# Kernel tuning notes

Measured on AMD Instinct MI355X. Metric: run time of the kernel, lower is better.

## Reference

```python
import jax, jax.numpy as jnp
import numpy as np

N_KV_HEADS = 8
MAX_CONTEXT = 8192
HEAD_DIM = 128  # dim // n_heads = 4096 // 32
N_NEW = 16


def setup_inputs() -> dict:
    key = jax.random.key(0)
    k1, k2, k3, k4, k5 = jax.random.split(key, 5)
    pos_ids = jnp.sort(jax.random.randint(k1, (N_NEW,), 0, MAX_CONTEXT, dtype=jnp.int64))
    k = jax.random.normal(k2, (1, N_KV_HEADS, N_NEW, HEAD_DIM), dtype=jnp.float32)
    v = jax.random.normal(k3, (1, N_KV_HEADS, N_NEW, HEAD_DIM), dtype=jnp.float32)
    k_cache = jax.random.normal(k4, (1, N_KV_HEADS, MAX_CONTEXT, HEAD_DIM), dtype=jnp.float32)
    v_cache = jax.random.normal(k5, (1, N_KV_HEADS, MAX_CONTEXT, HEAD_DIM), dtype=jnp.float32)
    return {"pos_ids": pos_ids, "k": k, "v": v, "k_cache": k_cache, "v_cache": v_cache}


def reference(pos_ids, k, v, k_cache, v_cache):
    # Functional equivalent of: clone cache, then cache[:, :, pos_ids, :] = new.
    # jnp .at[].set on the seq axis produces a fresh (copied) buffer, matching
    # the torch clone-then-scatter semantics.
    kout = k_cache.at[:, :, pos_ids, :].set(k)
    vout = v_cache.at[:, :, pos_ids, :].set(v)
    return (kout, vout)
```

## Files before the change

kernel.cpp:

```cpp
#include <hip/hip_runtime.h>


#define NNEW 16

typedef float f32x4 __attribute__((ext_vector_type(4)));

__global__ __launch_bounds__(256) void kv_copy_kernel(
    const f32x4* __restrict__ kcache,
    const f32x4* __restrict__ vcache,
    f32x4* __restrict__ out)
{
    const unsigned int i = blockIdx.x * 256u + threadIdx.x;
    const unsigned int j = i & ((1u << 21) - 1u);
    const f32x4* __restrict__ src = (i >> 21) ? vcache : kcache;
    f32x4 val = __builtin_nontemporal_load(&src[j]);
    __builtin_nontemporal_store(val, &out[i]);
}

__global__ __launch_bounds__(256) void kv_scatter_kernel(
    const int* __restrict__ pos,
    const f32x4* __restrict__ knew,
    const f32x4* __restrict__ vnew,
    f32x4* __restrict__ out)
{
    const unsigned int t  = blockIdx.x * 256u + threadIdx.x;
    const unsigned int d4 = t & 31u;
    const unsigned int n  = (t >> 5) & 15u;
    const unsigned int h  = (t >> 9) & 7u;
    const unsigned int c  = t >> 12;

    const int s = pos[n];

    bool skip = false;
#pragma unroll
    for (int m = 0; m < NNEW; ++m) {
        if (m > (int)n && pos[m] == s) skip = true;
    }
    if (skip) return;

    const f32x4* __restrict__ src = c ? vnew : knew;
    out[(c << 21) + (h << 18) + ((unsigned)s << 5) + d4] =
        src[(h * NNEW + n) * 32u + d4];
}

extern "C" void kernel_launch(void* const* d_in, const int* in_sizes, int n_in,
                              void* d_out, int out_size, void* d_ws, size_t ws_size,
                              hipStream_t stream) {
    const int*   pos    = (const int*)  d_in[0];
    const f32x4* knew   = (const f32x4*)d_in[1];
    const f32x4* vnew   = (const f32x4*)d_in[2];
    const f32x4* kcache = (const f32x4*)d_in[3];
    const f32x4* vcache = (const f32x4*)d_in[4];
    f32x4*       out    = (f32x4*)d_out;

    kv_copy_kernel<<<(1u << 22) / 256u, 256, 0, stream>>>(kcache, vcache, out);
    kv_scatter_kernel<<<8192 / 256, 256, 0, stream>>>(pos, knew, vnew, out);
}
```

Baseline: 128.3 us.

## Fuse cache copy and scatter into one kernel with per-row position lookup

Merges the bulk copy kernel and the scatter kernel into a single launch. Each thread owns four 16-byte chunks of one cache row, checks whether that row's sequence index matches any new position (the last match wins), and copies from either the new k/v or the old cache. This removes the second launch and avoids writing the new rows twice, but every thread now scans the 16-entry position list and the nontemporal load/store hints are dropped.

```diff
diff --git a/kernel.cpp b/kernel.cpp
--- a/kernel.cpp
+++ b/kernel.cpp
@@ -5,42 +5,48 @@
 
 typedef float f32x4 __attribute__((ext_vector_type(4)));
 
-__global__ __launch_bounds__(256) void kv_copy_kernel(
+__global__ __launch_bounds__(256) void kv_update_kernel(
+    const int* __restrict__ pos,
+    const f32x4* __restrict__ knew,
+    const f32x4* __restrict__ vnew,
     const f32x4* __restrict__ kcache,
     const f32x4* __restrict__ vcache,
     f32x4* __restrict__ out)
 {
-    const unsigned int i = blockIdx.x * 256u + threadIdx.x;
-    const unsigned int j = i & ((1u << 21) - 1u);
-    const f32x4* __restrict__ src = (i >> 21) ? vcache : kcache;
-    f32x4 val = __builtin_nontemporal_load(&src[j]);
-    __builtin_nontemporal_store(val, &out[i]);
-}
+    const unsigned int t  = blockIdx.x * 256u + threadIdx.x;
+    const unsigned int c  = t >> 19;
+    const unsigned int jb = t & ((1u << 19) - 1u);
+    const unsigned int r  = jb >> 3;
+    const unsigned int g  = jb & 7u;
+    const unsigned int h  = r >> 13;
+    const int          s  = (int)(r & 8191u);
 
-__global__ __launch_bounds__(256) void kv_scatter_kernel(
-    const int* __restrict__ pos,
-    const f32x4* __restrict__ knew,
-    const f32x4* __restrict__ vnew,
-    f32x4* __restrict__ out)
-{
-    const unsigned int t  = blockIdx.x * 256u + threadIdx.x;
-    const unsigned int d4 = t & 31u;
-    const unsigned int n  = (t >> 5) & 15u;
-    const unsigned int h  = (t >> 9) & 7u;
-    const unsigned int c  = t >> 12;
+    int match = -1;
+#pragma unroll
+    for (int n = 0; n < NNEW; ++n) {
+        if (pos[n] == s) match = n;
+    }
 
-    const int s = pos[n];
+    const f32x4* __restrict__ src;
+    unsigned int srcbase;
+    if (match >= 0) {
+        src = c ? vnew : knew;
+        srcbase = (h * NNEW + (unsigned)match) * 32u + g;
+    } else {
+        src = c ? vcache : kcache;
+        srcbase = r * 32u + g;
+    }
 
-    bool skip = false;
-#pragma unroll
-    for (int m = 0; m < NNEW; ++m) {
-        if (m > (int)n && pos[m] == s) skip = true;
-    }
-    if (skip) return;
+    const unsigned int outbase = (c << 21) + r * 32u + g;
 
-    const f32x4* __restrict__ src = c ? vnew : knew;
-    out[(c << 21) + (h << 18) + ((unsigned)s << 5) + d4] =
-        src[(h * NNEW + n) * 32u + d4];
+    f32x4 v0 = src[srcbase];
+    f32x4 v1 = src[srcbase + 8u];
+    f32x4 v2 = src[srcbase + 16u];
+    f32x4 v3 = src[srcbase + 24u];
+    out[outbase]       = v0;
+    out[outbase + 8u]  = v1;
+    out[outbase + 16u] = v2;
+    out[outbase + 24u] = v3;
 }
 
 extern "C" void kernel_launch(void* const* d_in, const int* in_sizes, int n_in,
@@ -53,6 +59,6 @@
     const f32x4* vcache = (const f32x4*)d_in[4];
     f32x4*       out    = (f32x4*)d_out;
 
-    kv_copy_kernel<<<(1u << 22) / 256u, 256, 0, stream>>>(kcache, vcache, out);
-    kv_scatter_kernel<<<8192 / 256, 256, 0, stream>>>(pos, knew, vnew, out);
+    kv_update_kernel<<<(1u << 20) / 256u, 256, 0, stream>>>(
+        pos, knew, vnew, kcache, vcache, out);
 }
```

Result: faster. 121.4 us (-5.4%).
